# Kernel optimization log

Hardware: AMD Instinct MI355X
Metric: run time of the kernel (lower is better)

Reference implementation:

```python
import jax, jax.numpy as jnp
import numpy as np
from jax import lax

EPS = 1e-4
DN = ('NDHWC', 'DHWIO', 'NDHWC')


def _m(mask, dtype):
    return mask[..., None].astype(dtype)


def bn_relu(x, mask):
    # BatchNorm1d over active voxels only (training-mode batch stats, gamma=1, beta=0), then ReLU.
    m = _m(mask, x.dtype)
    n = jnp.sum(m)
    mean = jnp.sum(x * m, axis=(0, 1, 2, 3)) / n
    xc = (x - mean) * m  # re-mask: inactive voxels stay exactly zero
    var = jnp.sum(xc * xc, axis=(0, 1, 2, 3)) / n
    return jnp.maximum(xc * lax.rsqrt(var + EPS), 0.0)


def subm3(x, w, mask):
    # SubMConv3d k=3 pad=1: dense conv on zero-at-inactive input, output restricted to active sites.
    y = lax.conv_general_dilated(x, w, (1, 1, 1), 'SAME', dimension_numbers=DN)
    return y * _m(mask, x.dtype)


def down2(x, w):
    # SparseConv3d k=2 s=2: non-overlapping windows; inactive inputs are zero so dense strided conv matches.
    return lax.conv_general_dilated(x, w, (2, 2, 2), 'VALID', dimension_numbers=DN)


def pool_mask(mask):
    B, D, H, W = mask.shape
    return jnp.any(mask.reshape(B, D // 2, 2, H // 2, 2, W // 2, 2), axis=(2, 4, 6))


def up2(x, w, mask):
    # SparseInverseConv3d k=2 (indice_key inverse of the stride-2 conv): conv-transpose masked to original indices.
    y = jnp.einsum('bdhwc,ijkco->bdihjwko', x, w)
    B, Dc, _, Hc, _, Wc, _, Co = y.shape
    return y.reshape(B, 2 * Dc, 2 * Hc, 2 * Wc, Co) * _m(mask, x.dtype)


def resblock(x, mask, wa, wb, w_sc=None):
    # ResidualBlock: i_branch (identity or 1x1 Custom1x1Subm3d: feats @ W.T) + BN-ReLU-SubM-BN-ReLU-SubM.
    idb = x if w_sc is None else jnp.einsum('bdhwc,oc->bdhwo', x, w_sc)
    h = bn_relu(x, mask)
    h = subm3(h, wa, mask)
    h = bn_relu(h, mask)
    h = subm3(h, wb, mask)
    return h + idb


def unet_forward(x, mask, w_in, w_b1a, w_b1b, w_d1, w_b2a, w_b2b, w_d2,
                 w_b3a, w_b3b, w_u2, w_t2_sc, w_t2a, w_t2b, w_u1, w_t1_sc, w_t1a, w_t1b):
    mask2 = pool_mask(mask)
    mask3 = pool_mask(mask2)
    x0 = subm3(x, w_in, mask)                 # input_conv (subm1)
    x1 = resblock(x0, mask, w_b1a, w_b1b)     # level-1 block (32->32)
    d1 = down2(bn_relu(x1, mask), w_d1)       # BN-ReLU + stride-2 conv 32->64
    x2 = resblock(d1, mask2, w_b2a, w_b2b)    # level-2 block (64->64)
    d2 = down2(bn_relu(x2, mask2), w_d2)      # 64->96
    x3 = resblock(d2, mask3, w_b3a, w_b3b)    # bottom level (96->96)
    u2 = up2(bn_relu(x3, mask3), w_u2, mask2)  # BN-ReLU + inverse conv 96->64
    t2 = resblock(jnp.concatenate([x2, u2], -1), mask2, w_t2a, w_t2b, w_t2_sc)  # tail 128->64
    u1 = up2(bn_relu(t2, mask2), w_u1, mask)   # 64->32
    t1 = resblock(jnp.concatenate([x1, u1], -1), mask, w_t1a, w_t1b, w_t1_sc)   # tail 64->32
    return bn_relu(t1, mask)                   # output_layer: BN + ReLU


def setup_inputs() -> dict:
    key = jax.random.key(0)
    ks = jax.random.split(key, 20)
    B, D = 1, 48
    Cin, C1, C2, C3 = 6, 32, 64, 96
    mask = jax.random.uniform(ks[0], (B, D, D, D)) < 0.12
    x = jax.random.normal(ks[1], (B, D, D, D, Cin), jnp.float32) * mask[..., None]

    def w(k, shape):
        fan = float(np.prod(shape[:-1]))
        return (jax.random.normal(k, shape, jnp.float32) / np.sqrt(fan)).astype(jnp.float32)

    return {
        'x': x, 'mask': mask,
        'w_in': w(ks[2], (3, 3, 3, Cin, C1)),
        'w_b1a': w(ks[3], (3, 3, 3, C1, C1)), 'w_b1b': w(ks[4], (3, 3, 3, C1, C1)),
        'w_d1': w(ks[5], (2, 2, 2, C1, C2)),
        'w_b2a': w(ks[6], (3, 3, 3, C2, C2)), 'w_b2b': w(ks[7], (3, 3, 3, C2, C2)),
        'w_d2': w(ks[8], (2, 2, 2, C2, C3)),
        'w_b3a': w(ks[9], (3, 3, 3, C3, C3)), 'w_b3b': w(ks[10], (3, 3, 3, C3, C3)),
        'w_u2': w(ks[11], (2, 2, 2, C3, C2)),
        'w_t2_sc': w(ks[12], (C2, 2 * C2)),
        'w_t2a': w(ks[13], (3, 3, 3, 2 * C2, C2)), 'w_t2b': w(ks[14], (3, 3, 3, C2, C2)),
        'w_u1': w(ks[15], (2, 2, 2, C2, C1)),
        'w_t1_sc': w(ks[16], (C1, 2 * C1)),
        'w_t1a': w(ks[17], (3, 3, 3, 2 * C1, C1)), 'w_t1b': w(ks[18], (3, 3, 3, C1, C1)),
    }


def reference(x, mask, w_in, w_b1a, w_b1b, w_d1, w_b2a, w_b2b, w_d2,
              w_b3a, w_b3b, w_u2, w_t2_sc, w_t2a, w_t2b, w_u1, w_t1_sc, w_t1a, w_t1b):
    return unet_forward(x, mask, w_in, w_b1a, w_b1b, w_d1, w_b2a, w_b2b, w_d2,
                        w_b3a, w_b3b, w_u2, w_t2_sc, w_t2a, w_t2b, w_u1, w_t1_sc, w_t1a, w_t1b)
```

## Files before the change

### kernel.cpp

```cpp
#include <hip/hip_runtime.h>


typedef short bf16x8 __attribute__((ext_vector_type(8)));
typedef float f32x4 __attribute__((ext_vector_type(4)));
typedef unsigned short ushort_t;

constexpr int D1 = 48, DIM2 = 24, DIM3 = 12;
constexpr int N1 = D1 * D1 * D1;
constexpr int N2 = DIM2 * DIM2 * DIM2;
constexpr int N3 = DIM3 * DIM3 * DIM3;

constexpr size_t OFF_A      = 0;
constexpr size_t OFF_R1     = 3538944;
constexpr size_t OFF_CAT1   = 7077888;
constexpr size_t OFF_D1R    = 14155776;
constexpr size_t OFF_R3     = 15040512;
constexpr size_t OFF_CAT2   = 15925248;
constexpr size_t OFF_D2R    = 17694720;
constexpr size_t OFF_R4     = 17860608;
constexpr size_t OFF_X3R    = 18026496;
constexpr size_t OFF_BN1_32 = 18192384;
constexpr size_t OFF_BN1_64 = 19961920;
constexpr size_t OFF_BN2_A  = 23500928;
constexpr size_t OFF_BN2_B  = 23943360;
constexpr size_t OFF_BN3_96 = 24385792;
constexpr size_t OFF_BFEND  = 24468800;
constexpr size_t OFF_WT     = 24468800;
constexpr size_t OFF_STATS  = 25142592;
constexpr size_t STATS_FLOATS = 16 * 4096;
constexpr size_t OFF_CNT    = OFF_STATS + STATS_FLOATS;
constexpr size_t OFF_L1     = OFF_CNT + 16;
constexpr size_t OFF_L2     = OFF_L1 + N1;
constexpr size_t OFF_L3     = OFF_L2 + N2;
constexpr size_t OFF_M1     = OFF_L3 + N3;
constexpr size_t OFF_M2     = OFF_M1 + N1 / 4;
constexpr size_t OFF_M3     = OFF_M2 + N2 / 4;

constexpr int WTS[17] = {0, 27648, 55296, 82944, 99328, 209920, 320512,
                         369664, 618496, 867328, 977920, 1088512, 1199104,
                         1254400, 1282048, 1331200, 1347584};

__device__ inline ushort_t f2bf(float f) {
  union { float f; unsigned u; } x; x.f = f;
  unsigned u = x.u + 0x7FFF + ((x.u >> 16) & 1);
  return (ushort_t)(u >> 16);
}

__global__ __launch_bounds__(256) void k_mask1(const float* __restrict__ x,
                                               unsigned char* __restrict__ m,
                                               int* __restrict__ list, int* __restrict__ cnt) {
  int v = blockIdx.x * 256 + threadIdx.x;
  if (v >= N1) return;
  const float* p = x + (size_t)v * 6;
  bool a = (p[0] != 0.f) || (p[1] != 0.f) || (p[2] != 0.f) ||
           (p[3] != 0.f) || (p[4] != 0.f) || (p[5] != 0.f);
  m[v] = a ? 1 : 0;
  if (a) { int pos = atomicAdd(cnt, 1); list[pos] = v; }
}

__global__ __launch_bounds__(256) void k_pool(const unsigned char* __restrict__ mf,
                                              unsigned char* __restrict__ mc,
                                              int* __restrict__ list, int* __restrict__ cnt, int DC) {
  int v = blockIdx.x * 256 + threadIdx.x;
  int n = DC * DC * DC;
  if (v >= n) return;
  int w = v % DC, h = (v / DC) % DC, d = v / (DC * DC);
  int DF = 2 * DC;
  bool a = false;
  for (int i = 0; i < 2; i++)
    for (int j = 0; j < 2; j++)
      for (int k = 0; k < 2; k++)
        a |= (mf[(size_t)(((2 * d + i) * DF + (2 * h + j)) * DF + (2 * w + k))] != 0);
  mc[v] = a ? 1 : 0;
  if (a) { int pos = atomicAdd(cnt, 1); list[pos] = v; }
}

struct WJobs {
  const float* src[16];
  int start[17];
  short cirtot[16], cio[16], cipad[16], cout[16];
};

__global__ __launch_bounds__(256) void k_wprep(WJobs jb, ushort_t* __restrict__ wt, int total) {
  int gid = blockIdx.x * 256 + threadIdx.x;
  if (gid >= total) return;
  int j = 0;
#pragma unroll
  for (int jj = 0; jj < 16; jj++)
    if (gid >= jb.start[jj + 1]) j = jj + 1;
  int e = gid - jb.start[j];
  int CIP = jb.cipad[j], CO = jb.cout[j];
  int CIRT = jb.cirtot[j], CIO = jb.cio[j];
  int ci = e % CIP;
  int co = (e / CIP) % CO;
  int k = e / (CIP * CO);
  float v = (ci + CIO < CIRT) ? jb.src[j][((size_t)k * CIRT + CIO + ci) * CO + co] : 0.f;
  wt[gid] = f2bf(v);
}

__global__ __launch_bounds__(256) void k_xprep(const float* __restrict__ x, ushort_t* __restrict__ xp) {
  int gid = blockIdx.x * 256 + threadIdx.x;
  if (gid >= (N1 + 4) * 8) return;
  int v = gid >> 3, c = (gid & 7) * 4;
  uint2 o = make_uint2(0u, 0u);
  if (v < N1) {
    ushort_t u[4];
#pragma unroll
    for (int j = 0; j < 4; j++) {
      int ci = c + j;
      float f = (ci < 6) ? x[(size_t)v * 6 + ci] : 0.f;
      u[j] = f2bf(f);
    }
    o.x = (unsigned)u[0] | ((unsigned)u[1] << 16);
    o.y = (unsigned)u[2] | ((unsigned)u[3] << 16);
  }
  *(uint2*)&xp[(size_t)v * 32 + c] = o;
}

template <int CIPAD, int CB, int KK, int DD, bool UP>
__global__ __launch_bounds__(512, 2) void k_conv7(
    const ushort_t* __restrict__ in, const ushort_t* __restrict__ wt, int cot,
    float* __restrict__ out, int ostride, int ooff,
    const float* __restrict__ res, int rstride,
    double* __restrict__ st,
    const int* __restrict__ list, const int* __restrict__ cnt) {
  constexpr int KCH = CIPAD / 32;
  constexpr int NCO = CB / 16;
  constexpr int TPS = (KK + 3) / 4;
  constexpr int BUNITS = KK * KCH * CB * 4;
  __shared__ ushort_t blds[BUNITS * 8];
  __shared__ float red[4][2][NCO * 4][64];
  __shared__ float sred0[CB], sred1[CB];
  __shared__ int vidx[32];

  int n = cnt[0];
  int t = threadIdx.x, wv = t >> 6, ln = t & 63;
  int vg = wv & 1, ks = wv >> 1;
  int fr = ln & 15, kg = ln >> 4;
  int coblk = blockIdx.y * CB;

  for (int e = t; e < BUNITS; e += 512) {
    int kgs = e & 3;
    int co = (e >> 2) % CB;
    int r2 = (e >> 2) / CB;
    int c = r2 % KCH;
    int k = r2 / KCH;
    bf16x8 w = *(const bf16x8*)(wt + ((size_t)k * cot + coblk + co) * CIPAD + c * 32 + kgs * 8);
    *(bf16x8*)(blds + (size_t)e * 8) = w;
  }
  if (t < CB) { sred0[t] = 0.f; sred1[t] = 0.f; }
  __syncthreads();

  float smr = 0.f, sqr = 0.f;
  int myco = ((t >> 8) % NCO) * 16 + (t & 15);

  for (int tile = blockIdx.x; tile * 32 < n; tile += gridDim.x) {
    int base = tile * 32;
    if (t < 32) vidx[t] = (base + t < n) ? list[base + t] : -1;
    __syncthreads();

    int av = vidx[vg * 16 + fr];
    int vv = av < 0 ? 0 : av;
    int ad = vv / (DD * DD), ah = (vv / DD) % DD, aw = vv % DD;
    int pidx = 0, corner = -1;
    if (UP) {
      constexpr int DC = DD / 2;
      pidx = (((ad >> 1) * DC) + (ah >> 1)) * DC + (aw >> 1);
      corner = ((ad & 1) << 2) | ((ah & 1) << 1) | (aw & 1);
    }
    constexpr int GDI = UP ? (DD / 2) : ((KK == 8) ? 2 * DD : DD);
    constexpr int SENT = GDI * GDI * GDI;

    const int k0 = ks * TPS;
    auto nixOf = [&](int kq) -> int {
      int kc = (kq < KK) ? kq : KK - 1;
      if (UP) {
        return (av >= 0 && corner == kc) ? pidx : SENT;
      } else if (KK == 27) {
        int kd = kc / 9 - 1, kh = (kc / 3) % 3 - 1, kw = kc % 3 - 1;
        int nd = ad + kd, nh = ah + kh, nw = aw + kw;
        bool inb = (av >= 0) && (unsigned)nd < (unsigned)DD &&
                   (unsigned)nh < (unsigned)DD && (unsigned)nw < (unsigned)DD;
        return inb ? (nd * DD + nh) * DD + nw : SENT;
      } else {
        return (av >= 0) ? ((2 * ad + ((kc >> 2) & 1)) * GDI + (2 * ah + ((kc >> 1) & 1))) * GDI +
                               (2 * aw + (kc & 1))
                         : SENT;
      }
    };
    auto loadA = [&](bf16x8* dst, int kq) {
      int nix = nixOf(kq);
      const ushort_t* ap = in + (size_t)nix * CIPAD + kg * 8;
#pragma unroll
      for (int c = 0; c < KCH; c++) dst[c] = *(const bf16x8*)(ap + c * 32);
    };

    f32x4 acc[NCO];
#pragma unroll
    for (int f = 0; f < NCO; f++) acc[f] = (f32x4){0.f, 0.f, 0.f, 0.f};

    bf16x8 aA[KCH], aB[KCH];
    loadA(aA, k0);
#pragma unroll
    for (int j = 0; j < TPS; j++) {
      bf16x8* cur = (j & 1) ? aB : aA;
      bf16x8* nxt = (j & 1) ? aA : aB;
      if (j + 1 < TPS) loadA(nxt, k0 + j + 1);
      if (k0 + j < KK) {
#pragma unroll
        for (int c = 0; c < KCH; c++) {
#pragma unroll
          for (int f = 0; f < NCO; f++) {
            bf16x8 b = *(const bf16x8*)(blds +
                ((((size_t)((k0 + j) * KCH + c) * CB) + f * 16 + fr) * 4 + kg) * 8);
            acc[f] = __builtin_amdgcn_mfma_f32_16x16x32_bf16(cur[c], b, acc[f], 0, 0, 0);
          }
        }
      }
    }

#pragma unroll
    for (int f = 0; f < NCO; f++)
#pragma unroll
      for (int r = 0; r < 4; r++)
        red[ks][vg][f * 4 + r][ln] = acc[f][r];
    __syncthreads();

#pragma unroll
    for (int e0 = 0; e0 < NCO; e0++) {
      int e = t + e0 * 512;
      int ln2 = e & 63, r = (e >> 6) & 3;
      int f = (e >> 8) % NCO;
      int vg2 = e / (256 * NCO);
      int ei = f * 4 + r;
      float s = red[0][vg2][ei][ln2] + red[1][vg2][ei][ln2] +
                red[2][vg2][ei][ln2] + red[3][vg2][ei][ln2];
      int slot = vg2 * 16 + (ln2 >> 4) * 4 + r;
      int co = f * 16 + (ln2 & 15);
      int v = vidx[slot];
      if (v >= 0) {
        int gco = coblk + co;
        float val = s;
        if (res) val += res[(size_t)v * rstride + gco];
        out[(size_t)v * ostride + ooff + gco] = val;
        smr += val; sqr += val * val;
      }
    }
    __syncthreads();
  }

  atomicAdd(&sred0[myco], smr);
  atomicAdd(&sred1[myco], sqr);
  __syncthreads();
  if (t < CB) {
    double* sr = st + (size_t)(blockIdx.x & 7) * 256;
    atomicAdd(&sr[coblk + t], (double)sred0[t]);
    atomicAdd(&sr[128 + coblk + t], (double)sred1[t]);
  }
}

template <int C>
__global__ __launch_bounds__(256) void k_bnapply2(
    const float* __restrict__ x, int xstr, int coff,
    const double* __restrict__ sA, const double* __restrict__ sB, int csplit,
    const int* __restrict__ list, const int* __restrict__ cnt,
    ushort_t* __restrict__ out) {
  __shared__ float mu_s[C], inv_s[C];
  int n = cnt[0];
  int t = threadIdx.x;
  if (t < C) {
    const double* s = (t < csplit) ? (sA + t) : (sB + (t - csplit));
    double sm = 0.0, sq = 0.0;
#pragma unroll
    for (int r = 0; r < 8; r++) { sm += s[r * 256]; sq += s[r * 256 + 128]; }
    double mu = sm / n;
    double var = sq / n - mu * mu;
    mu_s[t] = (float)mu;
    inv_s[t] = rsqrtf((float)fmax(var, 0.0) + 1e-4f);
  }
  __syncthreads();
  int total = n * (C / 4);
  for (int gid = blockIdx.x * 256 + t; gid < total; gid += gridDim.x * 256) {
    int i = gid / (C / 4);
    int c = (gid % (C / 4)) * 4;
    int v = list[i];
    float4 xv = *(const float4*)&x[(size_t)v * xstr + coff + c];
    float xa[4] = {xv.x, xv.y, xv.z, xv.w};
    ushort_t u[4];
#pragma unroll
    for (int j = 0; j < 4; j++)
      u[j] = f2bf(fmaxf((xa[j] - mu_s[c + j]) * inv_s[c + j], 0.f));
    uint2 o; o.x = (unsigned)u[0] | ((unsigned)u[1] << 16);
    o.y = (unsigned)u[2] | ((unsigned)u[3] << 16);
    *(uint2*)&out[(size_t)v * C + c] = o;
  }
}

__global__ __launch_bounds__(256) void k_bnout(const float* __restrict__ x,
                                               const unsigned char* __restrict__ m,
                                               const double* __restrict__ s,
                                               const int* __restrict__ cnt,
                                               float* __restrict__ out) {
  __shared__ float mu_s[32], inv_s[32];
  int t = threadIdx.x;
  int n = cnt[0];
  if (t < 32) {
    double sm = 0.0, sq = 0.0;
#pragma unroll
    for (int r = 0; r < 8; r++) { sm += s[r * 256 + t]; sq += s[r * 256 + 128 + t]; }
    double mu = sm / n;
    double var = sq / n - mu * mu;
    mu_s[t] = (float)mu;
    inv_s[t] = rsqrtf((float)fmax(var, 0.0) + 1e-4f);
  }
  __syncthreads();
  int gid = blockIdx.x * 256 + t;
  if (gid >= N1 * 8) return;
  int v = gid / 8;
  int c = (gid % 8) * 4;
  float4 o = make_float4(0.f, 0.f, 0.f, 0.f);
  if (m[v]) {
    float4 xv = *(const float4*)&x[(size_t)v * 32 + c];
    o.x = fmaxf((xv.x - mu_s[c + 0]) * inv_s[c + 0], 0.f);
    o.y = fmaxf((xv.y - mu_s[c + 1]) * inv_s[c + 1], 0.f);
    o.z = fmaxf((xv.z - mu_s[c + 2]) * inv_s[c + 2], 0.f);
    o.w = fmaxf((xv.w - mu_s[c + 3]) * inv_s[c + 3], 0.f);
  }
  *(float4*)&out[(size_t)v * 32 + c] = o;
}

template <int CI, int CO>
__global__ __launch_bounds__(256) void k_sc(const float* __restrict__ in,
                                            const float* __restrict__ wsc,
                                            float* __restrict__ out,
                                            const int* __restrict__ list,
                                            const int* __restrict__ cnt) {
  int n = cnt[0];
  long total = (long)n * CO;
  for (long gid = (long)blockIdx.x * 256 + threadIdx.x; gid < total; gid += (long)gridDim.x * 256) {
    int i = (int)(gid / CO), o = (int)(gid % CO);
    int v = list[i];
    const float4* xr = (const float4*)(in + (size_t)v * CI);
    const float4* wr = (const float4*)(wsc + (size_t)o * CI);
    float a = 0.f;
    for (int c = 0; c < CI / 4; c++) {
      float4 x4 = xr[c], w4 = wr[c];
      a += x4.x * w4.x + x4.y * w4.y + x4.z * w4.z + x4.w * w4.w;
    }
    out[(size_t)v * CO + o] = a;
  }
}

extern "C" void kernel_launch(void* const* d_in, const int* in_sizes, int n_in,
                              void* d_out, int out_size, void* d_ws, size_t ws_size,
                              hipStream_t stream) {
  float* W = (float*)d_ws;
  const float* x = (const float*)d_in[0];

  float* A    = W + OFF_A;
  float* R1   = W + OFF_R1;
  float* CAT1 = W + OFF_CAT1;
  float* D1R  = W + OFF_D1R;
  float* R3   = W + OFF_R3;
  float* CAT2 = W + OFF_CAT2;
  float* D2R  = W + OFF_D2R;
  float* R4   = W + OFF_R4;
  float* X3R  = W + OFF_X3R;
  ushort_t* XP     = (ushort_t*)(W + OFF_CAT1);
  ushort_t* BN1_32 = (ushort_t*)(W + OFF_BN1_32);
  ushort_t* BN1_64 = (ushort_t*)(W + OFF_BN1_64);
  ushort_t* BN2A   = (ushort_t*)(W + OFF_BN2_A);
  ushort_t* BN2B   = (ushort_t*)(W + OFF_BN2_B);
  ushort_t* BN3_96 = (ushort_t*)(W + OFF_BN3_96);
  ushort_t* WT  = (ushort_t*)(W + OFF_WT);
  double* S0 = (double*)(W + OFF_STATS);
  int* CNT = (int*)(W + OFF_CNT);
  int* L1 = (int*)(W + OFF_L1);
  int* L2 = (int*)(W + OFF_L2);
  int* L3 = (int*)(W + OFF_L3);
  unsigned char* M1 = (unsigned char*)(W + OFF_M1);
  unsigned char* M2 = (unsigned char*)(W + OFF_M2);
  unsigned char* M3 = (unsigned char*)(W + OFF_M3);

  auto S = [&](int i) { return S0 + (size_t)i * 2048; };

  hipMemsetAsync(W + OFF_STATS, 0, (STATS_FLOATS + 16) * 4, stream);
  hipMemsetAsync(W + OFF_BN1_32, 0, (OFF_BFEND - OFF_BN1_32) * 4, stream);

  k_mask1<<<N1 / 256, 256, 0, stream>>>(x, M1, L1, CNT + 0);
  k_pool<<<N2 / 256, 256, 0, stream>>>(M1, M2, L2, CNT + 1, DIM2);
  k_pool<<<(N3 + 255) / 256, 256, 0, stream>>>(M2, M3, L3, CNT + 2, DIM3);

  WJobs jb;
  const int srcIdx[16]  = {2, 3, 4, 5, 6, 7, 8, 9, 10, 13, 13, 14, 17, 18, 11, 15};
  const short cirtot[16]= {6, 32, 32, 32, 64, 64, 64, 96, 96, 128, 128, 64, 64, 32, 96, 64};
  const short cio[16]   = {0, 0, 0, 0, 0, 0, 0, 0, 0, 0, 64, 0, 0, 0, 0, 0};
  const short cipad[16] = {32, 32, 32, 32, 64, 64, 64, 96, 96, 64, 64, 64, 64, 32, 96, 64};
  const short couts[16] = {32, 32, 32, 64, 64, 64, 96, 96, 96, 64, 64, 64, 32, 32, 64, 32};
  for (int j = 0; j < 16; j++) {
    jb.src[j] = (const float*)d_in[srcIdx[j]];
    jb.cirtot[j] = cirtot[j]; jb.cio[j] = cio[j];
    jb.cipad[j] = cipad[j]; jb.cout[j] = couts[j];
    jb.start[j] = WTS[j];
  }
  jb.start[16] = WTS[16];
  k_wprep<<<(WTS[16] + 255) / 256, 256, 0, stream>>>(jb, WT, WTS[16]);
  k_xprep<<<((N1 + 4) * 8 + 255) / 256, 256, 0, stream>>>(x, XP);

  const int BNG = 512;

  k_conv7<32, 32, 27, D1, false><<<dim3(256, 1), 512, 0, stream>>>(
      XP, WT + WTS[0], 32, A, 32, 0, nullptr, 0, S(0), L1, CNT + 0);
  k_bnapply2<32><<<BNG, 256, 0, stream>>>(A, 32, 0, S(0), S(0), 32, L1, CNT + 0, BN1_32);
  k_conv7<32, 32, 27, D1, false><<<dim3(256, 1), 512, 0, stream>>>(
      BN1_32, WT + WTS[1], 32, R1, 32, 0, nullptr, 0, S(1), L1, CNT + 0);
  k_bnapply2<32><<<BNG, 256, 0, stream>>>(R1, 32, 0, S(1), S(1), 32, L1, CNT + 0, BN1_32);
  k_conv7<32, 32, 27, D1, false><<<dim3(256, 1), 512, 0, stream>>>(
      BN1_32, WT + WTS[2], 32, CAT1, 64, 0, A, 32, S(2), L1, CNT + 0);
  k_bnapply2<32><<<BNG, 256, 0, stream>>>(CAT1, 64, 0, S(2), S(2), 32, L1, CNT + 0, BN1_32);
  k_conv7<32, 32, 8, DIM2, false><<<dim3(128, 2), 512, 0, stream>>>(
      BN1_32, WT + WTS[3], 64, D1R, 64, 0, nullptr, 0, S(3), L2, CNT + 1);

  k_bnapply2<64><<<BNG, 256, 0, stream>>>(D1R, 64, 0, S(3), S(3), 64, L2, CNT + 1, BN2A);
  k_conv7<64, 32, 27, DIM2, false><<<dim3(128, 2), 512, 0, stream>>>(
      BN2A, WT + WTS[4], 64, R3, 64, 0, nullptr, 0, S(4), L2, CNT + 1);
  k_bnapply2<64><<<BNG, 256, 0, stream>>>(R3, 64, 0, S(4), S(4), 64, L2, CNT + 1, BN2A);
  k_conv7<64, 32, 27, DIM2, false><<<dim3(128, 2), 512, 0, stream>>>(
      BN2A, WT + WTS[5], 64, CAT2, 128, 0, D1R, 64, S(5), L2, CNT + 1);
  k_bnapply2<64><<<BNG, 256, 0, stream>>>(CAT2, 128, 0, S(5), S(5), 64, L2, CNT + 1, BN2A);
  k_conv7<64, 32, 8, DIM3, false><<<dim3(54, 3), 512, 0, stream>>>(
      BN2A, WT + WTS[6], 96, D2R, 96, 0, nullptr, 0, S(6), L3, CNT + 2);

  k_bnapply2<96><<<BNG, 256, 0, stream>>>(D2R, 96, 0, S(6), S(6), 96, L3, CNT + 2, BN3_96);
  k_conv7<96, 16, 27, DIM3, false><<<dim3(54, 6), 512, 0, stream>>>(
      BN3_96, WT + WTS[7], 96, R4, 96, 0, nullptr, 0, S(7), L3, CNT + 2);
  k_bnapply2<96><<<BNG, 256, 0, stream>>>(R4, 96, 0, S(7), S(7), 96, L3, CNT + 2, BN3_96);
  k_conv7<96, 16, 27, DIM3, false><<<dim3(54, 6), 512, 0, stream>>>(
      BN3_96, WT + WTS[8], 96, X3R, 96, 0, D2R, 96, S(8), L3, CNT + 2);
  k_bnapply2<96><<<BNG, 256, 0, stream>>>(X3R, 96, 0, S(8), S(8), 96, L3, CNT + 2, BN3_96);
  k_conv7<96, 32, 8, DIM2, true><<<dim3(128, 2), 512, 0, stream>>>(
      BN3_96, WT + WTS[14], 64, CAT2, 128, 64, nullptr, 0, S(9), L2, CNT + 1);

  k_bnapply2<64><<<BNG, 256, 0, stream>>>(CAT2, 128, 64, S(9), S(9), 64, L2, CNT + 1, BN2B);
  k_conv7<64, 32, 27, DIM2, false><<<dim3(128, 2), 512, 0, stream>>>(
      BN2A, WT + WTS[9], 64, R3, 64, 0, nullptr, 0, S(15), L2, CNT + 1);
  k_conv7<64, 32, 27, DIM2, false><<<dim3(128, 2), 512, 0, stream>>>(
      BN2B, WT + WTS[10], 64, R3, 64, 0, R3, 64, S(10), L2, CNT + 1);
  k_bnapply2<64><<<BNG, 256, 0, stream>>>(R3, 64, 0, S(10), S(10), 64, L2, CNT + 1, BN2A);
  k_sc<128, 64><<<512, 256, 0, stream>>>(CAT2, (const float*)d_in[12], D1R, L2, CNT + 1);
  k_conv7<64, 32, 27, DIM2, false><<<dim3(128, 2), 512, 0, stream>>>(
      BN2A, WT + WTS[11], 64, R3, 64, 0, D1R, 64, S(11), L2, CNT + 1);
  k_bnapply2<64><<<BNG, 256, 0, stream>>>(R3, 64, 0, S(11), S(11), 64, L2, CNT + 1, BN2A);
  k_conv7<64, 32, 8, D1, true><<<dim3(256, 1), 512, 0, stream>>>(
      BN2A, WT + WTS[15], 32, CAT1, 64, 32, nullptr, 0, S(12), L1, CNT + 0);

  k_bnapply2<64><<<BNG, 256, 0, stream>>>(CAT1, 64, 0, S(2), S(12), 32, L1, CNT + 0, BN1_64);
  k_conv7<64, 32, 27, D1, false><<<dim3(256, 1), 512, 0, stream>>>(
      BN1_64, WT + WTS[12], 32, R1, 32, 0, nullptr, 0, S(13), L1, CNT + 0);
  k_bnapply2<32><<<BNG, 256, 0, stream>>>(R1, 32, 0, S(13), S(13), 32, L1, CNT + 0, BN1_32);
  k_sc<64, 32><<<512, 256, 0, stream>>>(CAT1, (const float*)d_in[16], A, L1, CNT + 0);
  k_conv7<32, 32, 27, D1, false><<<dim3(256, 1), 512, 0, stream>>>(
      BN1_32, WT + WTS[13], 32, A, 32, 0, A, 32, S(14), L1, CNT + 0);
  k_bnout<<<N1 * 8 / 256, 256, 0, stream>>>(A, M1, S(14), CNT + 0, (float*)d_out);
}
```

Baseline: 391.6 us.

## Fuse BN-ReLU and bf16 conversion into conv gather; fuse shortcut into conv epilogue

Removes the separate bn-apply kernels. Each conv now reads fp32 activations, computes BN mean and inverse std from the stats in its prologue, and applies normalize, ReLU and mask before packing to bf16 for MFMA. The 1x1 shortcut matmul moves into the conv epilogue, and the mask, list and weight prep kernels merge into one prep kernel. The LDS weight layout gets a padded stride, and several convs switch to 16-wide output blocks with more y-blocks. In exchange, gathers are fp32 (twice the bytes), normalization is redone for every one of the 27 taps, and there is an extra mask lookup per tap.

```diff
diff --git a/kernel.cpp b/kernel.cpp
--- a/kernel.cpp
+++ b/kernel.cpp
@@ -10,35 +10,32 @@
 constexpr int N2 = DIM2 * DIM2 * DIM2;
 constexpr int N3 = DIM3 * DIM3 * DIM3;
 
-constexpr size_t OFF_A      = 0;
-constexpr size_t OFF_R1     = 3538944;
-constexpr size_t OFF_CAT1   = 7077888;
-constexpr size_t OFF_D1R    = 14155776;
-constexpr size_t OFF_R3     = 15040512;
-constexpr size_t OFF_CAT2   = 15925248;
-constexpr size_t OFF_D2R    = 17694720;
-constexpr size_t OFF_R4     = 17860608;
-constexpr size_t OFF_X3R    = 18026496;
-constexpr size_t OFF_BN1_32 = 18192384;
-constexpr size_t OFF_BN1_64 = 19961920;
-constexpr size_t OFF_BN2_A  = 23500928;
-constexpr size_t OFF_BN2_B  = 23943360;
-constexpr size_t OFF_BN3_96 = 24385792;
-constexpr size_t OFF_BFEND  = 24468800;
-constexpr size_t OFF_WT     = 24468800;
-constexpr size_t OFF_STATS  = 25142592;
+constexpr size_t OFF_A    = 0;
+constexpr size_t OFF_R1   = 3538944;
+constexpr size_t OFF_CAT1 = 7077888;
+constexpr size_t OFF_T1R  = 14155776;
+constexpr size_t OFF_D1R  = 17694720;
+constexpr size_t OFF_R3   = 18579456;
+constexpr size_t OFF_CAT2 = 19464192;
+constexpr size_t OFF_T2R  = 21233664;
+constexpr size_t OFF_D2R  = 22118400;
+constexpr size_t OFF_R4   = 22284288;
+constexpr size_t OFF_X3R  = 22450176;
+constexpr size_t OFF_WT   = 22616064;
+constexpr size_t OFF_STATS= 23289856;
 constexpr size_t STATS_FLOATS = 16 * 4096;
-constexpr size_t OFF_CNT    = OFF_STATS + STATS_FLOATS;
-constexpr size_t OFF_L1     = OFF_CNT + 16;
-constexpr size_t OFF_L2     = OFF_L1 + N1;
-constexpr size_t OFF_L3     = OFF_L2 + N2;
-constexpr size_t OFF_M1     = OFF_L3 + N3;
-constexpr size_t OFF_M2     = OFF_M1 + N1 / 4;
-constexpr size_t OFF_M3     = OFF_M2 + N2 / 4;
+constexpr size_t OFF_CNT  = OFF_STATS + STATS_FLOATS;
+constexpr size_t OFF_L1   = OFF_CNT + 16;
+constexpr size_t OFF_L2   = OFF_L1 + N1;
+constexpr size_t OFF_L3   = OFF_L2 + N2;
+constexpr size_t OFF_M1   = OFF_L3 + N3;
+constexpr size_t OFF_M2   = OFF_M1 + N1 / 4;
+constexpr size_t OFF_M3   = OFF_M2 + N2 / 4;
 
 constexpr int WTS[17] = {0, 27648, 55296, 82944, 99328, 209920, 320512,
                          369664, 618496, 867328, 977920, 1088512, 1199104,
                          1254400, 1282048, 1331200, 1347584};
+constexpr int WTOT = 1347584;
 
 __device__ inline ushort_t f2bf(float f) {
   union { float f; unsigned u; } x; x.f = f;
@@ -46,16 +43,38 @@
   return (ushort_t)(u >> 16);
 }
 
-__global__ __launch_bounds__(256) void k_mask1(const float* __restrict__ x,
-                                               unsigned char* __restrict__ m,
-                                               int* __restrict__ list, int* __restrict__ cnt) {
-  int v = blockIdx.x * 256 + threadIdx.x;
-  if (v >= N1) return;
-  const float* p = x + (size_t)v * 6;
-  bool a = (p[0] != 0.f) || (p[1] != 0.f) || (p[2] != 0.f) ||
-           (p[3] != 0.f) || (p[4] != 0.f) || (p[5] != 0.f);
-  m[v] = a ? 1 : 0;
-  if (a) { int pos = atomicAdd(cnt, 1); list[pos] = v; }
+struct WJobs {
+  const float* src[16];
+  int start[17];
+  short cirtot[16], cio[16], cipad[16], cout[16];
+};
+
+__global__ __launch_bounds__(256) void k_prep(WJobs jb, const float* __restrict__ x,
+                                              unsigned char* __restrict__ m,
+                                              int* __restrict__ list, int* __restrict__ cnt,
+                                              ushort_t* __restrict__ wt) {
+  int gid = blockIdx.x * 256 + threadIdx.x;
+  int gs = gridDim.x * 256;
+  for (int v = gid; v < N1; v += gs) {
+    const float* p = x + (size_t)v * 6;
+    bool a = (p[0] != 0.f) || (p[1] != 0.f) || (p[2] != 0.f) ||
+             (p[3] != 0.f) || (p[4] != 0.f) || (p[5] != 0.f);
+    m[v] = a ? 1 : 0;
+    if (a) { int pos = atomicAdd(cnt, 1); list[pos] = v; }
+  }
+  for (int e = gid; e < WTOT; e += gs) {
+    int j = 0;
+#pragma unroll
+    for (int jj = 0; jj < 16; jj++)
+      if (e >= jb.start[jj + 1]) j = jj + 1;
+    int le = e - jb.start[j];
+    int CIP = jb.cipad[j], CO = jb.cout[j], CIRT = jb.cirtot[j], CIO = jb.cio[j];
+    int ci = le % CIP;
+    int co = (le / CIP) % CO;
+    int k = le / (CIP * CO);
+    float v = (ci + CIO < CIRT) ? jb.src[j][((size_t)k * CIRT + CIO + ci) * CO + co] : 0.f;
+    wt[e] = f2bf(v);
+  }
 }
 
 __global__ __launch_bounds__(256) void k_pool(const unsigned char* __restrict__ mf,
@@ -75,84 +94,73 @@
   if (a) { int pos = atomicAdd(cnt, 1); list[pos] = v; }
 }
 
-struct WJobs {
-  const float* src[16];
-  int start[17];
-  short cirtot[16], cio[16], cipad[16], cout[16];
-};
-
-__global__ __launch_bounds__(256) void k_wprep(WJobs jb, ushort_t* __restrict__ wt, int total) {
-  int gid = blockIdx.x * 256 + threadIdx.x;
-  if (gid >= total) return;
-  int j = 0;
-#pragma unroll
-  for (int jj = 0; jj < 16; jj++)
-    if (gid >= jb.start[jj + 1]) j = jj + 1;
-  int e = gid - jb.start[j];
-  int CIP = jb.cipad[j], CO = jb.cout[j];
-  int CIRT = jb.cirtot[j], CIO = jb.cio[j];
-  int ci = e % CIP;
-  int co = (e / CIP) % CO;
-  int k = e / (CIP * CO);
-  float v = (ci + CIO < CIRT) ? jb.src[j][((size_t)k * CIRT + CIO + ci) * CO + co] : 0.f;
-  wt[gid] = f2bf(v);
-}
-
-__global__ __launch_bounds__(256) void k_xprep(const float* __restrict__ x, ushort_t* __restrict__ xp) {
-  int gid = blockIdx.x * 256 + threadIdx.x;
-  if (gid >= (N1 + 4) * 8) return;
-  int v = gid >> 3, c = (gid & 7) * 4;
-  uint2 o = make_uint2(0u, 0u);
-  if (v < N1) {
-    ushort_t u[4];
-#pragma unroll
-    for (int j = 0; j < 4; j++) {
-      int ci = c + j;
-      float f = (ci < 6) ? x[(size_t)v * 6 + ci] : 0.f;
-      u[j] = f2bf(f);
-    }
-    o.x = (unsigned)u[0] | ((unsigned)u[1] << 16);
-    o.y = (unsigned)u[2] | ((unsigned)u[3] << 16);
-  }
-  *(uint2*)&xp[(size_t)v * 32 + c] = o;
-}
-
-template <int CIPAD, int CB, int KK, int DD, bool UP>
-__global__ __launch_bounds__(512, 2) void k_conv7(
-    const ushort_t* __restrict__ in, const ushort_t* __restrict__ wt, int cot,
-    float* __restrict__ out, int ostride, int ooff,
-    const float* __restrict__ res, int rstride,
-    double* __restrict__ st,
-    const int* __restrict__ list, const int* __restrict__ cnt) {
+template <int CIPAD, int CB, int KK, int DD, bool UP, bool NORM, int CIRAW, int SCCI>
+__global__ __launch_bounds__(512) void k_conv10(
+    const float* __restrict__ in, int istr, int icoff,
+    const int* __restrict__ cntIn,
+    const ushort_t* __restrict__ wt, int cot,
+    const unsigned char* __restrict__ msk,
+    const double* __restrict__ stA, const double* __restrict__ stB, int csplit,
+    float* __restrict__ out, int ostr, int ooff,
+    const float* __restrict__ res, int rstr,
+    const float* __restrict__ scIn, const float* __restrict__ scW,
+    double* __restrict__ stOut,
+    const int* __restrict__ list, const int* __restrict__ cntOut) {
   constexpr int KCH = CIPAD / 32;
   constexpr int NCO = CB / 16;
   constexpr int TPS = (KK + 3) / 4;
-  constexpr int BUNITS = KK * KCH * CB * 4;
-  __shared__ ushort_t blds[BUNITS * 8];
+  constexpr int CBP = CB + 1;
+  constexpr int ETOT = 2 * NCO * 256;
+  constexpr int NE = ETOT / 512;
+  __shared__ ushort_t blds[KK * KCH * 4 * CBP * 8];
   __shared__ float red[4][2][NCO * 4][64];
-  __shared__ float sred0[CB], sred1[CB];
+  __shared__ float s_iv[CIPAD], s_mv[CIPAD];
+  __shared__ float sred[2 * CB];
   __shared__ int vidx[32];
 
-  int n = cnt[0];
-  int t = threadIdx.x, wv = t >> 6, ln = t & 63;
-  int vg = wv & 1, ks = wv >> 1;
-  int fr = ln & 15, kg = ln >> 4;
-  int coblk = blockIdx.y * CB;
-
-  for (int e = t; e < BUNITS; e += 512) {
-    int kgs = e & 3;
-    int co = (e >> 2) % CB;
-    int r2 = (e >> 2) / CB;
-    int c = r2 % KCH;
-    int k = r2 / KCH;
-    bf16x8 w = *(const bf16x8*)(wt + ((size_t)k * cot + coblk + co) * CIPAD + c * 32 + kgs * 8);
-    *(bf16x8*)(blds + (size_t)e * 8) = w;
-  }
-  if (t < CB) { sred0[t] = 0.f; sred1[t] = 0.f; }
+  const int n = cntOut[0];
+  const int t = threadIdx.x, wv = t >> 6, ln = t & 63;
+  const int vg = wv & 1, ks = wv >> 1;
+  const int fr = ln & 15, kg = ln >> 4;
+  const int coblk = blockIdx.y * CB;
+  const int k0 = ks * TPS;
+
+  for (int e = t; e < KK * KCH * 4 * CB; e += 512) {
+    int co = e % CB;
+    int r2 = e / CB;
+    int kgs = r2 & 3, r3 = r2 >> 2;
+    int c = r3 % KCH, k = r3 / KCH;
+    *(bf16x8*)(blds + ((size_t)r2 * CBP + co) * 8) =
+        *(const bf16x8*)(wt + ((size_t)k * cot + coblk + co) * CIPAD + c * 32 + kgs * 8);
+  }
+  if (NORM && t < CIPAD) {
+    int nIn = cntIn[0];
+    const double* s = (t < csplit) ? (stA + t) : (stB + (t - csplit));
+    double sm = 0.0, sq = 0.0;
+#pragma unroll
+    for (int r = 0; r < 8; r++) { sm += s[r * 256]; sq += s[r * 256 + 128]; }
+    double mu = sm / nIn, var = sq / nIn - mu * mu;
+    float iv = rsqrtf((float)fmax(var, 0.0) + 1e-4f);
+    s_iv[t] = iv;
+    s_mv[t] = (float)mu * iv;
+  }
+  if (t < 2 * CB) sred[t] = 0.f;
   __syncthreads();
 
+  float ivv[KCH][8], mvv[KCH][8];
+  if (NORM) {
+#pragma unroll
+    for (int c = 0; c < KCH; c++)
+#pragma unroll
+      for (int q = 0; q < 8; q++) {
+        int ch = c * 32 + kg * 8 + q;
+        ivv[c][q] = s_iv[ch];
+        mvv[c][q] = s_mv[ch];
+      }
+  }
+
   float smr = 0.f, sqr = 0.f;
-  int myco = ((t >> 8) % NCO) * 16 + (t & 15);
+  constexpr int GDI = UP ? (DD / 2) : ((KK == 8) ? 2 * DD : DD);
 
   for (int tile = blockIdx.x; tile * 32 < n; tile += gridDim.x) {
     int base = tile * 32;
@@ -168,52 +176,79 @@
       pidx = (((ad >> 1) * DC) + (ah >> 1)) * DC + (aw >> 1);
       corner = ((ad & 1) << 2) | ((ah & 1) << 1) | (aw & 1);
     }
-    constexpr int GDI = UP ? (DD / 2) : ((KK == 8) ? 2 * DD : DD);
-    constexpr int SENT = GDI * GDI * GDI;
-
-    const int k0 = ks * TPS;
-    auto nixOf = [&](int kq) -> int {
-      int kc = (kq < KK) ? kq : KK - 1;
+
+    float aF[2][KCH][8];
+    float okf[2];
+
+    auto LOADT = [&](int st, int j) {
+      int k = k0 + j;
+      bool ok;
+      int nix;
       if (UP) {
-        return (av >= 0 && corner == kc) ? pidx : SENT;
+        ok = (av >= 0) && (corner == k);
+        nix = ok ? pidx : 0;
       } else if (KK == 27) {
+        int kc = (k < KK) ? k : KK - 1;
         int kd = kc / 9 - 1, kh = (kc / 3) % 3 - 1, kw = kc % 3 - 1;
         int nd = ad + kd, nh = ah + kh, nw = aw + kw;
-        bool inb = (av >= 0) && (unsigned)nd < (unsigned)DD &&
-                   (unsigned)nh < (unsigned)DD && (unsigned)nw < (unsigned)DD;
-        return inb ? (nd * DD + nh) * DD + nw : SENT;
+        ok = (k < KK) && (av >= 0) && ((unsigned)nd < (unsigned)DD) &&
+             ((unsigned)nh < (unsigned)DD) && ((unsigned)nw < (unsigned)DD);
+        nix = ok ? (nd * DD + nh) * DD + nw : 0;
       } else {
-        return (av >= 0) ? ((2 * ad + ((kc >> 2) & 1)) * GDI + (2 * ah + ((kc >> 1) & 1))) * GDI +
-                               (2 * aw + (kc & 1))
-                         : SENT;
+        int kd = (k >> 2) & 1, kh = (k >> 1) & 1, kw = k & 1;
+        ok = (av >= 0);
+        nix = ok ? ((2 * ad + kd) * GDI + (2 * ah + kh)) * GDI + (2 * aw + kw) : 0;
+      }
+      if (NORM && msk) ok = ok && (msk[nix] != 0);
+      okf[st] = ok ? 1.f : 0.f;
+      if (CIRAW == 6) {
+        if (kg == 0) {
+          const float* ap = in + (size_t)nix * 6;
+          aF[st][0][0] = ap[0]; aF[st][0][1] = ap[1]; aF[st][0][2] = ap[2];
+          aF[st][0][3] = ap[3]; aF[st][0][4] = ap[4]; aF[st][0][5] = ap[5];
+          aF[st][0][6] = 0.f;   aF[st][0][7] = 0.f;
+        } else {
+#pragma unroll
+          for (int q = 0; q < 8; q++) aF[st][0][q] = 0.f;
+        }
+      } else {
+#pragma unroll
+        for (int c = 0; c < KCH; c++) {
+          const float* ap = in + (size_t)nix * istr + icoff + c * 32 + kg * 8;
+          float4 u0 = *(const float4*)ap;
+          float4 u1 = *(const float4*)(ap + 4);
+          aF[st][c][0] = u0.x; aF[st][c][1] = u0.y; aF[st][c][2] = u0.z; aF[st][c][3] = u0.w;
+          aF[st][c][4] = u1.x; aF[st][c][5] = u1.y; aF[st][c][6] = u1.z; aF[st][c][7] = u1.w;
+        }
       }
     };
-    auto loadA = [&](bf16x8* dst, int kq) {
-      int nix = nixOf(kq);
-      const ushort_t* ap = in + (size_t)nix * CIPAD + kg * 8;
-#pragma unroll
-      for (int c = 0; c < KCH; c++) dst[c] = *(const bf16x8*)(ap + c * 32);
-    };
 
     f32x4 acc[NCO];
 #pragma unroll
     for (int f = 0; f < NCO; f++) acc[f] = (f32x4){0.f, 0.f, 0.f, 0.f};
 
-    bf16x8 aA[KCH], aB[KCH];
-    loadA(aA, k0);
+    LOADT(0, 0);
 #pragma unroll
     for (int j = 0; j < TPS; j++) {
-      bf16x8* cur = (j & 1) ? aB : aA;
-      bf16x8* nxt = (j & 1) ? aA : aB;
-      if (j + 1 < TPS) loadA(nxt, k0 + j + 1);
+      if (j + 1 < TPS) LOADT((j + 1) & 1, j + 1);
       if (k0 + j < KK) {
+        const int st = j & 1;
 #pragma unroll
         for (int c = 0; c < KCH; c++) {
+          bf16x8 afr;
+#pragma unroll
+          for (int q = 0; q < 8; q++) {
+            float xq = aF[st][c][q];
+            float y;
+            if (NORM) y = fmaxf(fmaf(xq, ivv[c][q], -mvv[c][q]), 0.f) * okf[st];
+            else      y = xq * okf[st];
+            afr[q] = (short)f2bf(y);
+          }
 #pragma unroll
           for (int f = 0; f < NCO; f++) {
             bf16x8 b = *(const bf16x8*)(blds +
-                ((((size_t)((k0 + j) * KCH + c) * CB) + f * 16 + fr) * 4 + kg) * 8);
-            acc[f] = __builtin_amdgcn_mfma_f32_16x16x32_bf16(cur[c], b, acc[f], 0, 0, 0);
+                ((size_t)(((k0 + j) * KCH + c) * 4 + kg) * CBP + f * 16 + fr) * 8);
+            acc[f] = __builtin_amdgcn_mfma_f32_16x16x32_bf16(afr, b, acc[f], 0, 0, 0);
           }
         }
       }
@@ -227,72 +262,50 @@
     __syncthreads();
 
 #pragma unroll
-    for (int e0 = 0; e0 < NCO; e0++) {
+    for (int e0 = 0; e0 < NE; e0++) {
       int e = t + e0 * 512;
       int ln2 = e & 63, r = (e >> 6) & 3;
       int f = (e >> 8) % NCO;
       int vg2 = e / (256 * NCO);
-      int ei = f * 4 + r;
-      float s = red[0][vg2][ei][ln2] + red[1][vg2][ei][ln2] +
-                red[2][vg2][ei][ln2] + red[3][vg2][ei][ln2];
+      float sv = red[0][vg2][f * 4 + r][ln2] + red[1][vg2][f * 4 + r][ln2] +
+                 red[2][vg2][f * 4 + r][ln2] + red[3][vg2][f * 4 + r][ln2];
       int slot = vg2 * 16 + (ln2 >> 4) * 4 + r;
-      int co = f * 16 + (ln2 & 15);
-      int v = vidx[slot];
+      int ii = base + slot;
+      int v = (ii < n) ? list[ii] : -1;
       if (v >= 0) {
-        int gco = coblk + co;
-        float val = s;
-        if (res) val += res[(size_t)v * rstride + gco];
-        out[(size_t)v * ostride + ooff + gco] = val;
-        smr += val; sqr += val * val;
+        int gco = coblk + f * 16 + (ln2 & 15);
+        float val = sv;
+        if (SCCI > 0) {
+          const float4* xr = (const float4*)(scIn + (size_t)v * SCCI);
+          const float4* wq = (const float4*)(scW + (size_t)gco * SCCI);
+          float a = 0.f;
+#pragma unroll 8
+          for (int c = 0; c < SCCI / 4; c++) {
+            float4 xv = xr[c], wv_ = wq[c];
+            a += xv.x * wv_.x + xv.y * wv_.y + xv.z * wv_.z + xv.w * wv_.w;
+          }
+          val += a;
+        } else if (res) {
+          val += res[(size_t)v * rstr + gco];
+        }
+        out[(size_t)v * ostr + ooff + gco] = val;
+        smr += val;
+        sqr += val * val;
       }
     }
     __syncthreads();
   }
 
-  atomicAdd(&sred0[myco], smr);
-  atomicAdd(&sred1[myco], sqr);
+  {
+    int myco = ((t >> 8) % NCO) * 16 + (t & 15);
+    atomicAdd(&sred[myco], smr);
+    atomicAdd(&sred[CB + myco], sqr);
+  }
   __syncthreads();
   if (t < CB) {
-    double* sr = st + (size_t)(blockIdx.x & 7) * 256;
-    atomicAdd(&sr[coblk + t], (double)sred0[t]);
-    atomicAdd(&sr[128 + coblk + t], (double)sred1[t]);
-  }
-}
-
-template <int C>
-__global__ __launch_bounds__(256) void k_bnapply2(
-    const float* __restrict__ x, int xstr, int coff,
-    const double* __restrict__ sA, const double* __restrict__ sB, int csplit,
-    const int* __restrict__ list, const int* __restrict__ cnt,
-    ushort_t* __restrict__ out) {
-  __shared__ float mu_s[C], inv_s[C];
-  int n = cnt[0];
-  int t = threadIdx.x;
-  if (t < C) {
-    const double* s = (t < csplit) ? (sA + t) : (sB + (t - csplit));
-    double sm = 0.0, sq = 0.0;
-#pragma unroll
-    for (int r = 0; r < 8; r++) { sm += s[r * 256]; sq += s[r * 256 + 128]; }
-    double mu = sm / n;
-    double var = sq / n - mu * mu;
-    mu_s[t] = (float)mu;
-    inv_s[t] = rsqrtf((float)fmax(var, 0.0) + 1e-4f);
-  }
-  __syncthreads();
-  int total = n * (C / 4);
-  for (int gid = blockIdx.x * 256 + t; gid < total; gid += gridDim.x * 256) {
-    int i = gid / (C / 4);
-    int c = (gid % (C / 4)) * 4;
-    int v = list[i];
-    float4 xv = *(const float4*)&x[(size_t)v * xstr + coff + c];
-    float xa[4] = {xv.x, xv.y, xv.z, xv.w};
-    ushort_t u[4];
-#pragma unroll
-    for (int j = 0; j < 4; j++)
-      u[j] = f2bf(fmaxf((xa[j] - mu_s[c + j]) * inv_s[c + j], 0.f));
-    uint2 o; o.x = (unsigned)u[0] | ((unsigned)u[1] << 16);
-    o.y = (unsigned)u[2] | ((unsigned)u[3] << 16);
-    *(uint2*)&out[(size_t)v * C + c] = o;
+    double* sr = stOut + (size_t)((int)blockIdx.x & 7) * 256;
+    atomicAdd(&sr[coblk + t], (double)sred[t]);
+    atomicAdd(&sr[128 + coblk + t], (double)sred[CB + t]);
   }
 }
 
@@ -310,8 +323,9 @@
     for (int r = 0; r < 8; r++) { sm += s[r * 256 + t]; sq += s[r * 256 + 128 + t]; }
     double mu = sm / n;
     double var = sq / n - mu * mu;
-    mu_s[t] = (float)mu;
-    inv_s[t] = rsqrtf((float)fmax(var, 0.0) + 1e-4f);
+    float iv = rsqrtf((float)fmax(var, 0.0) + 1e-4f);
+    mu_s[t] = (float)mu * iv;
+    inv_s[t] = iv;
   }
   __syncthreads();
   int gid = blockIdx.x * 256 + t;
@@ -321,34 +335,12 @@
   float4 o = make_float4(0.f, 0.f, 0.f, 0.f);
   if (m[v]) {
     float4 xv = *(const float4*)&x[(size_t)v * 32 + c];
-    o.x = fmaxf((xv.x - mu_s[c + 0]) * inv_s[c + 0], 0.f);
-    o.y = fmaxf((xv.y - mu_s[c + 1]) * inv_s[c + 1], 0.f);
-    o.z = fmaxf((xv.z - mu_s[c + 2]) * inv_s[c + 2], 0.f);
-    o.w = fmaxf((xv.w - mu_s[c + 3]) * inv_s[c + 3], 0.f);
+    o.x = fmaxf(fmaf(xv.x, inv_s[c + 0], -mu_s[c + 0]), 0.f);
+    o.y = fmaxf(fmaf(xv.y, inv_s[c + 1], -mu_s[c + 1]), 0.f);
+    o.z = fmaxf(fmaf(xv.z, inv_s[c + 2], -mu_s[c + 2]), 0.f);
+    o.w = fmaxf(fmaf(xv.w, inv_s[c + 3], -mu_s[c + 3]), 0.f);
   }
   *(float4*)&out[(size_t)v * 32 + c] = o;
-}
-
-template <int CI, int CO>
-__global__ __launch_bounds__(256) void k_sc(const float* __restrict__ in,
-                                            const float* __restrict__ wsc,
-                                            float* __restrict__ out,
-                                            const int* __restrict__ list,
-                                            const int* __restrict__ cnt) {
-  int n = cnt[0];
-  long total = (long)n * CO;
-  for (long gid = (long)blockIdx.x * 256 + threadIdx.x; gid < total; gid += (long)gridDim.x * 256) {
-    int i = (int)(gid / CO), o = (int)(gid % CO);
-    int v = list[i];
-    const float4* xr = (const float4*)(in + (size_t)v * CI);
-    const float4* wr = (const float4*)(wsc + (size_t)o * CI);
-    float a = 0.f;
-    for (int c = 0; c < CI / 4; c++) {
-      float4 x4 = xr[c], w4 = wr[c];
-      a += x4.x * w4.x + x4.y * w4.y + x4.z * w4.z + x4.w * w4.w;
-    }
-    out[(size_t)v * CO + o] = a;
-  }
 }
 
 extern "C" void kernel_launch(void* const* d_in, const int* in_sizes, int n_in,
@@ -360,19 +352,15 @@
   float* A    = W + OFF_A;
   float* R1   = W + OFF_R1;
   float* CAT1 = W + OFF_CAT1;
+  float* T1R  = W + OFF_T1R;
   float* D1R  = W + OFF_D1R;
   float* R3   = W + OFF_R3;
   float* CAT2 = W + OFF_CAT2;
+  float* T2R  = W + OFF_T2R;
   float* D2R  = W + OFF_D2R;
   float* R4   = W + OFF_R4;
   float* X3R  = W + OFF_X3R;
-  ushort_t* XP     = (ushort_t*)(W + OFF_CAT1);
-  ushort_t* BN1_32 = (ushort_t*)(W + OFF_BN1_32);
-  ushort_t* BN1_64 = (ushort_t*)(W + OFF_BN1_64);
-  ushort_t* BN2A   = (ushort_t*)(W + OFF_BN2_A);
-  ushort_t* BN2B   = (ushort_t*)(W + OFF_BN2_B);
-  ushort_t* BN3_96 = (ushort_t*)(W + OFF_BN3_96);
-  ushort_t* WT  = (ushort_t*)(W + OFF_WT);
+  ushort_t* WT = (ushort_t*)(W + OFF_WT);
   double* S0 = (double*)(W + OFF_STATS);
   int* CNT = (int*)(W + OFF_CNT);
   int* L1 = (int*)(W + OFF_L1);
@@ -381,15 +369,12 @@
   unsigned char* M1 = (unsigned char*)(W + OFF_M1);
   unsigned char* M2 = (unsigned char*)(W + OFF_M2);
   unsigned char* M3 = (unsigned char*)(W + OFF_M3);
+  const float* wsc2 = (const float*)d_in[12];
+  const float* wsc1 = (const float*)d_in[16];
 
   auto S = [&](int i) { return S0 + (size_t)i * 2048; };
 
   hipMemsetAsync(W + OFF_STATS, 0, (STATS_FLOATS + 16) * 4, stream);
-  hipMemsetAsync(W + OFF_BN1_32, 0, (OFF_BFEND - OFF_BN1_32) * 4, stream);
-
-  k_mask1<<<N1 / 256, 256, 0, stream>>>(x, M1, L1, CNT + 0);
-  k_pool<<<N2 / 256, 256, 0, stream>>>(M1, M2, L2, CNT + 1, DIM2);
-  k_pool<<<(N3 + 255) / 256, 256, 0, stream>>>(M2, M3, L3, CNT + 2, DIM3);
 
   WJobs jb;
   const int srcIdx[16]  = {2, 3, 4, 5, 6, 7, 8, 9, 10, 13, 13, 14, 17, 18, 11, 15};
@@ -404,62 +389,63 @@
     jb.start[j] = WTS[j];
   }
   jb.start[16] = WTS[16];
-  k_wprep<<<(WTS[16] + 255) / 256, 256, 0, stream>>>(jb, WT, WTS[16]);
-  k_xprep<<<((N1 + 4) * 8 + 255) / 256, 256, 0, stream>>>(x, XP);
-
-  const int BNG = 512;
-
-  k_conv7<32, 32, 27, D1, false><<<dim3(256, 1), 512, 0, stream>>>(
-      XP, WT + WTS[0], 32, A, 32, 0, nullptr, 0, S(0), L1, CNT + 0);
-  k_bnapply2<32><<<BNG, 256, 0, stream>>>(A, 32, 0, S(0), S(0), 32, L1, CNT + 0, BN1_32);
-  k_conv7<32, 32, 27, D1, false><<<dim3(256, 1), 512, 0, stream>>>(
-      BN1_32, WT + WTS[1], 32, R1, 32, 0, nullptr, 0, S(1), L1, CNT + 0);
-  k_bnapply2<32><<<BNG, 256, 0, stream>>>(R1, 32, 0, S(1), S(1), 32, L1, CNT + 0, BN1_32);
-  k_conv7<32, 32, 27, D1, false><<<dim3(256, 1), 512, 0, stream>>>(
-      BN1_32, WT + WTS[2], 32, CAT1, 64, 0, A, 32, S(2), L1, CNT + 0);
-  k_bnapply2<32><<<BNG, 256, 0, stream>>>(CAT1, 64, 0, S(2), S(2), 32, L1, CNT + 0, BN1_32);
-  k_conv7<32, 32, 8, DIM2, false><<<dim3(128, 2), 512, 0, stream>>>(
-      BN1_32, WT + WTS[3], 64, D1R, 64, 0, nullptr, 0, S(3), L2, CNT + 1);
-
-  k_bnapply2<64><<<BNG, 256, 0, stream>>>(D1R, 64, 0, S(3), S(3), 64, L2, CNT + 1, BN2A);
-  k_conv7<64, 32, 27, DIM2, false><<<dim3(128, 2), 512, 0, stream>>>(
-      BN2A, WT + WTS[4], 64, R3, 64, 0, nullptr, 0, S(4), L2, CNT + 1);
-  k_bnapply2<64><<<BNG, 256, 0, stream>>>(R3, 64, 0, S(4), S(4), 64, L2, CNT + 1, BN2A);
-  k_conv7<64, 32, 27, DIM2, false><<<dim3(128, 2), 512, 0, stream>>>(
-      BN2A, WT + WTS[5], 64, CAT2, 128, 0, D1R, 64, S(5), L2, CNT + 1);
-  k_bnapply2<64><<<BNG, 256, 0, stream>>>(CAT2, 128, 0, S(5), S(5), 64, L2, CNT + 1, BN2A);
-  k_conv7<64, 32, 8, DIM3, false><<<dim3(54, 3), 512, 0, stream>>>(
-      BN2A, WT + WTS[6], 96, D2R, 96, 0, nullptr, 0, S(6), L3, CNT + 2);
-
-  k_bnapply2<96><<<BNG, 256, 0, stream>>>(D2R, 96, 0, S(6), S(6), 96, L3, CNT + 2, BN3_96);
-  k_conv7<96, 16, 27, DIM3, false><<<dim3(54, 6), 512, 0, stream>>>(
-      BN3_96, WT + WTS[7], 96, R4, 96, 0, nullptr, 0, S(7), L3, CNT + 2);
-  k_bnapply2<96><<<BNG, 256, 0, stream>>>(R4, 96, 0, S(7), S(7), 96, L3, CNT + 2, BN3_96);
-  k_conv7<96, 16, 27, DIM3, false><<<dim3(54, 6), 512, 0, stream>>>(
-      BN3_96, WT + WTS[8], 96, X3R, 96, 0, D2R, 96, S(8), L3, CNT + 2);
-  k_bnapply2<96><<<BNG, 256, 0, stream>>>(X3R, 96, 0, S(8), S(8), 96, L3, CNT + 2, BN3_96);
-  k_conv7<96, 32, 8, DIM2, true><<<dim3(128, 2), 512, 0, stream>>>(
-      BN3_96, WT + WTS[14], 64, CAT2, 128, 64, nullptr, 0, S(9), L2, CNT + 1);
-
-  k_bnapply2<64><<<BNG, 256, 0, stream>>>(CAT2, 128, 64, S(9), S(9), 64, L2, CNT + 1, BN2B);
-  k_conv7<64, 32, 27, DIM2, false><<<dim3(128, 2), 512, 0, stream>>>(
-      BN2A, WT + WTS[9], 64, R3, 64, 0, nullptr, 0, S(15), L2, CNT + 1);
-  k_conv7<64, 32, 27, DIM2, false><<<dim3(128, 2), 512, 0, stream>>>(
-      BN2B, WT + WTS[10], 64, R3, 64, 0, R3, 64, S(10), L2, CNT + 1);
-  k_bnapply2<64><<<BNG, 256, 0, stream>>>(R3, 64, 0, S(10), S(10), 64, L2, CNT + 1, BN2A);
-  k_sc<128, 64><<<512, 256, 0, stream>>>(CAT2, (const float*)d_in[12], D1R, L2, CNT + 1);
-  k_conv7<64, 32, 27, DIM2, false><<<dim3(128, 2), 512, 0, stream>>>(
-      BN2A, WT + WTS[11], 64, R3, 64, 0, D1R, 64, S(11), L2, CNT + 1);
-  k_bnapply2<64><<<BNG, 256, 0, stream>>>(R3, 64, 0, S(11), S(11), 64, L2, CNT + 1, BN2A);
-  k_conv7<64, 32, 8, D1, true><<<dim3(256, 1), 512, 0, stream>>>(
-      BN2A, WT + WTS[15], 32, CAT1, 64, 32, nullptr, 0, S(12), L1, CNT + 0);
-
-  k_bnapply2<64><<<BNG, 256, 0, stream>>>(CAT1, 64, 0, S(2), S(12), 32, L1, CNT + 0, BN1_64);
-  k_conv7<64, 32, 27, D1, false><<<dim3(256, 1), 512, 0, stream>>>(
-      BN1_64, WT + WTS[12], 32, R1, 32, 0, nullptr, 0, S(13), L1, CNT + 0);
-  k_bnapply2<32><<<BNG, 256, 0, stream>>>(R1, 32, 0, S(13), S(13), 32, L1, CNT + 0, BN1_32);
-  k_sc<64, 32><<<512, 256, 0, stream>>>(CAT1, (const float*)d_in[16], A, L1, CNT + 0);
-  k_conv7<32, 32, 27, D1, false><<<dim3(256, 1), 512, 0, stream>>>(
-      BN1_32, WT + WTS[13], 32, A, 32, 0, A, 32, S(14), L1, CNT + 0);
-  k_bnout<<<N1 * 8 / 256, 256, 0, stream>>>(A, M1, S(14), CNT + 0, (float*)d_out);
-}
+
+  k_prep<<<864, 256, 0, stream>>>(jb, x, M1, L1, CNT + 0, WT);
+  k_pool<<<N2 / 256, 256, 0, stream>>>(M1, M2, L2, CNT + 1, DIM2);
+  k_pool<<<(N3 + 255) / 256, 256, 0, stream>>>(M2, M3, L3, CNT + 2, DIM3);
+
+  k_conv10<32, 32, 27, D1, false, false, 6, 0><<<dim3(256, 1), 512, 0, stream>>>(
+      x, 6, 0, CNT + 0, WT + WTS[0], 32, nullptr, S(0), S(0), 32,
+      A, 32, 0, nullptr, 0, nullptr, nullptr, S(0), L1, CNT + 0);
+  k_conv10<32, 32, 27, D1, false, true, 0, 0><<<dim3(256, 1), 512, 0, stream>>>(
+      A, 32, 0, CNT + 0, WT + WTS[1], 32, M1, S(0), S(0), 32,
+      R1, 32, 0, nullptr, 0, nullptr, nullptr, S(1), L1, CNT + 0);
+  k_conv10<32, 32, 27, D1, false, true, 0, 0><<<dim3(256, 1), 512, 0, stream>>>(
+      R1, 32, 0, CNT + 0, WT + WTS[2], 32, M1, S(1), S(1), 32,
+      CAT1, 64, 0, A, 32, nullptr, nullptr, S(2), L1, CNT + 0);
+  k_conv10<32, 32, 8, DIM2, false, true, 0, 0><<<dim3(128, 2), 512, 0, stream>>>(
+      CAT1, 64, 0, CNT + 0, WT + WTS[3], 64, M1, S(2), S(2), 32,
+      D1R, 64, 0, nullptr, 0, nullptr, nullptr, S(3), L2, CNT + 1);
+
+  k_conv10<64, 16, 27, DIM2, false, true, 0, 0><<<dim3(64, 4), 512, 0, stream>>>(
+      D1R, 64, 0, CNT + 1, WT + WTS[4], 64, M2, S(3), S(3), 64,
+      R3, 64, 0, nullptr, 0, nullptr, nullptr, S(4), L2, CNT + 1);
+  k_conv10<64, 16, 27, DIM2, false, true, 0, 0><<<dim3(64, 4), 512, 0, stream>>>(
+      R3, 64, 0, CNT + 1, WT + WTS[5], 64, M2, S(4), S(4), 64,
+      CAT2, 128, 0, D1R, 64, nullptr, nullptr, S(5), L2, CNT + 1);
+  k_conv10<64, 32, 8, DIM3, false, true, 0, 0><<<dim3(54, 3), 512, 0, stream>>>(
+      CAT2, 128, 0, CNT + 1, WT + WTS[6], 96, M2, S(5), S(5), 64,
+      D2R, 96, 0, nullptr, 0, nullptr, nullptr, S(6), L3, CNT + 2);
+
+  k_conv10<96, 16, 27, DIM3, false, true, 0, 0><<<dim3(54, 6), 512, 0, stream>>>(
+      D2R, 96, 0, CNT + 2, WT + WTS[7], 96, M3, S(6), S(6), 96,
+      R4, 96, 0, nullptr, 0, nullptr, nullptr, S(7), L3, CNT + 2);
+  k_conv10<96, 16, 27, DIM3, false, true, 0, 0><<<dim3(54, 6), 512, 0, stream>>>(
+      R4, 96, 0, CNT + 2, WT + WTS[8], 96, M3, S(7), S(7), 96,
+      X3R, 96, 0, D2R, 96, nullptr, nullptr, S(8), L3, CNT + 2);
+  k_conv10<96, 32, 8, DIM2, true, true, 0, 0><<<dim3(128, 2), 512, 0, stream>>>(
+      X3R, 96, 0, CNT + 2, WT + WTS[14], 64, nullptr, S(8), S(8), 96,
+      CAT2, 128, 64, nullptr, 0, nullptr, nullptr, S(9), L2, CNT + 1);
+
+  k_conv10<64, 16, 27, DIM2, false, true, 0, 0><<<dim3(64, 4), 512, 0, stream>>>(
+      CAT2, 128, 0, CNT + 1, WT + WTS[9], 64, M2, S(5), S(5), 64,
+      R3, 64, 0, nullptr, 0, nullptr, nullptr, S(15), L2, CNT + 1);
+  k_conv10<64, 16, 27, DIM2, false, true, 0, 0><<<dim3(64, 4), 512, 0, stream>>>(
+      CAT2, 128, 64, CNT + 1, WT + WTS[10], 64, M2, S(9), S(9), 64,
+      R3, 64, 0, R3, 64, nullptr, nullptr, S(10), L2, CNT + 1);
+  k_conv10<64, 16, 27, DIM2, false, true, 0, 128><<<dim3(64, 4), 512, 0, stream>>>(
+      R3, 64, 0, CNT + 1, WT + WTS[11], 64, M2, S(10), S(10), 64,
+      T2R, 64, 0, nullptr, 0, CAT2, wsc2, S(11), L2, CNT + 1);
+  k_conv10<64, 32, 8, D1, true, true, 0, 0><<<dim3(256, 1), 512, 0, stream>>>(
+      T2R, 64, 0, CNT + 1, WT + WTS[15], 32, nullptr, S(11), S(11), 64,
+      CAT1, 64, 32, nullptr, 0, nullptr, nullptr, S(12), L1, CNT + 0);
+
+  k_conv10<64, 16, 27, D1, false, true, 0, 0><<<dim3(128, 2), 512, 0, stream>>>(
+      CAT1, 64, 0, CNT + 0, WT + WTS[12], 32, M1, S(2), S(12), 32,
+      R1, 32, 0, nullptr, 0, nullptr, nullptr, S(13), L1, CNT + 0);
+  k_conv10<32, 32, 27, D1, false, true, 0, 64><<<dim3(256, 1), 512, 0, stream>>>(
+      R1, 32, 0, CNT + 0, WT + WTS[13], 32, M1, S(13), S(13), 32,
+      T1R, 32, 0, nullptr, 0, CAT1, wsc1, S(14), L1, CNT + 0);
+
+  k_bnout<<<N1 * 8 / 256, 256, 0, stream>>>(T1R, M1, S(14), CNT + 0, (float*)d_out);
+}
```

Result: slower. 551.7 us (+40.9%).
